# Kernel tuning notes

Hardware: AMD Instinct MI355X
Metric: run time of the kernel (lower is better)

Reference implementation:

```python
import jax, jax.numpy as jnp
import numpy as np

OBS_LEN = 8
N_PED = 2048      # total pedestrians
G = 64            # number of scenes (uniform size)
NP = N_PED // G   # pedestrians per scene = 32
H = 128           # action_decoder_hidden_dim == action_encoder_hidden_dim == f_in == f_out
DIN = 64          # action_encoder_input_dim
DD = 64           # distance_embedding_dim
NH = 4            # n_heads (hard-coded to 4 in GAT)


def setup_inputs() -> dict:
    key = jax.random.key(0)
    ks = jax.random.split(key, 16)
    s = 0.1  # weight scale (xavier-ish)
    starts = (jnp.arange(G) * NP).astype(jnp.int64)
    seq_start_end = jnp.stack([starts, starts + NP], axis=1)
    return {
        "obs_traj": jax.random.normal(ks[0], (OBS_LEN, N_PED, 2), jnp.float32),
        "goal_hidden_state": jax.random.normal(ks[1], (N_PED, H), jnp.float32),
        "goal": jax.random.normal(ks[2], (N_PED, 2), jnp.float32),
        "action": jax.random.normal(ks[3], (N_PED, 2), jnp.float32),
        "h0": jax.random.normal(ks[4], (N_PED, H), jnp.float32),
        "c0": jax.random.normal(ks[5], (N_PED, H), jnp.float32),
        "W_emb": jax.random.normal(ks[6], (2, DIN), jnp.float32) * s,
        "b_emb": jnp.zeros((DIN,), jnp.float32),
        "W_ih": jax.random.normal(ks[7], (4 * H, DIN), jnp.float32) * s,
        "W_hh": jax.random.normal(ks[8], (4 * H, H), jnp.float32) * s,
        "b_ih": jnp.zeros((4 * H,), jnp.float32),
        "b_hh": jnp.zeros((4 * H,), jnp.float32),
        "W_dist": jax.random.normal(ks[9], (8, DD), jnp.float32) * s,
        "b_dist": jnp.zeros((DD,), jnp.float32),
        "W_gate": jax.random.normal(ks[10], (DD, H), jnp.float32) * s,
        "b_gate": jnp.zeros((H,), jnp.float32),
        "gat_w": jax.random.normal(ks[11], (NH, 1, H, H), jnp.float32) * s,
        "gat_a": jax.random.normal(ks[12], (1, 1, 2 * H, 1), jnp.float32) * s,
        "gat_bias": jnp.zeros((H,), jnp.float32),
        "seq_start_end": seq_start_end,
    }


def _forward(obs_traj, goal_hidden_state, goal, action, h0, c0,
             W_emb, b_emb, W_ih, W_hh, b_ih, b_hh,
             W_dist, b_dist, W_gate, b_gate, gat_w, gat_a, gat_bias,
             seq_start_end):
    T, N, _ = obs_traj.shape
    g_num = seq_start_end.shape[0]
    n = N // g_num  # uniform group size

    # --- ActionEncoder: embed + LSTMCell loop over obs_len (lax.scan) ---
    x = jax.nn.relu(obs_traj.reshape(-1, 2) @ W_emb + b_emb).reshape(T, N, -1)

    def lstm_step(carry, xt):
        h, c = carry
        gates = xt @ W_ih.T + b_ih + h @ W_hh.T + b_hh  # torch gate order i,f,g,o
        i, f, g, o = jnp.split(gates, 4, axis=-1)
        c = jax.nn.sigmoid(f) * c + jax.nn.sigmoid(i) * jnp.tanh(g)
        h = jax.nn.sigmoid(o) * jnp.tanh(c)
        return (h, c), None

    (action_hidden, _), _ = jax.lax.scan(lstm_step, (h0, c0), x)  # [N, H]

    Hd = action_hidden.shape[-1]
    ahg = action_hidden.reshape(g_num, n, Hd)
    ghg = goal_hidden_state.reshape(g_num, n, Hd)
    glg = goal.reshape(g_num, n, 2)
    acg = action.reshape(g_num, n, 2)

    eye = jnp.eye(n, dtype=action_hidden.dtype)[:, :, None]  # [n, n, 1]

    def gat_group(ah, gh, gl, ac):
        # InteractionGate.cal_gate: dist[i,j] = [action_i, goal_i, action_j, goal_j]
        a_i = jnp.broadcast_to(ac[:, None, :], (n, n, 2))
        g_i = jnp.broadcast_to(gl[:, None, :], (n, n, 2))
        a_j = jnp.broadcast_to(ac[None, :, :], (n, n, 2))
        g_j = jnp.broadcast_to(gl[None, :, :], (n, n, 2))
        dist = jnp.concatenate([a_i, g_i, a_j, g_j], axis=-1)  # [n, n, 8]
        gate = jax.nn.sigmoid(jax.nn.relu(dist @ W_dist + b_dist) @ W_gate + b_gate)  # [n, n, H]

        # gate_action[i,j] = gate[i,j] * tanh(action_hidden[j])
        gate_action = gate * jnp.tanh(ah[None, :, :])
        # diagonal -> goal_hidden[i], off-diag -> gated action
        goal_action = eye * gh[None, :, :] + (1.0 - eye) * gate_action  # [n, n, H]

        h_other = jnp.concatenate([ah[:, None, :], goal_action], axis=1)  # [n, n+1, H]
        h_self = jnp.broadcast_to(ah[:, None, :], (n, n + 1, Hd))          # [n, n+1, H]

        # GraphAttentionLayer
        w = gat_w[:, 0]  # [NH, H, H]
        hs = jnp.einsum('nkf,hfo->hnko', h_self, w)   # [NH, n, n+1, H]
        ho = jnp.einsum('nkf,hfo->hnko', h_other, w)  # [NH, n, n+1, H]
        scores = jnp.concatenate([hs, ho], axis=-1) @ gat_a[0, 0, :, 0]  # [NH, n, n+1]
        alpha = jax.nn.softmax(jax.nn.leaky_relu(scores, 0.2), axis=-1)
        out = jnp.mean(jnp.sum(alpha[..., None] * ho, axis=2), axis=0)  # [n, H]
        return jax.nn.relu(out) + gat_bias

    out = jax.vmap(gat_group)(ahg, ghg, glg, acg)  # [G, n, H]
    return out.reshape(N, Hd)


def reference(obs_traj, goal_hidden_state, goal, action, h0, c0,
              W_emb, b_emb, W_ih, W_hh, b_ih, b_hh,
              W_dist, b_dist, W_gate, b_gate, gat_w, gat_a, gat_bias,
              seq_start_end):
    return _forward(obs_traj, goal_hidden_state, goal, action, h0, c0,
                    W_emb, b_emb, W_ih, W_hh, b_ih, b_hh,
                    W_dist, b_dist, W_gate, b_gate, gat_w, gat_a, gat_bias,
                    seq_start_end)
```

## Files before the change

kernel.cpp:

```cpp
#include <hip/hip_runtime.h>

#define N_PED 2048
#define NGROUP 64
#define NPG 32
#define HDIM 128
#define DIN 64
#define DDIM 64
#define NHEAD 4
#define TOBS 8

typedef __attribute__((ext_vector_type(8))) short bf16x8;
typedef __attribute__((ext_vector_type(4))) float f32x4;

__device__ __forceinline__ float sigm(float x){
    return __builtin_amdgcn_rcpf(1.f + __expf(-x));
}
__device__ __forceinline__ float tanh_fast(float x){
    return 1.f - 2.f*__builtin_amdgcn_rcpf(__expf(2.f*x) + 1.f);
}
__device__ __forceinline__ short f2bf(float f){
    unsigned u = __float_as_uint(f);
    unsigned r = (u + 0x7fffu + ((u >> 16) & 1u)) >> 16;
    return (short)r;
}
__device__ __forceinline__ float bf2f(unsigned short b){
    return __uint_as_float(((unsigned)b) << 16);
}
__device__ __forceinline__ unsigned pk2(float a, float b){
    return (unsigned)(unsigned short)f2bf(a) | ((unsigned)(unsigned short)f2bf(b) << 16);
}

#define WS_AHB   0
#define WS_TAHB  524288
#define WS_VW    1048576
#define WS_GF    1052672
#define WS_WF    1069056
#define WS_LF    1200128
#define WS_BSV   1396736

__global__ __launch_bounds__(512) void pack_lstm_kernel(
    const float* __restrict__ W_ih,  const float* __restrict__ W_hh,
    const float* __restrict__ b_ih,  const float* __restrict__ b_hh,
    unsigned char* __restrict__ ws)
{
    const int tid = threadIdx.x;
    const int b   = blockIdx.x;
    if (b < 24) {
        const int id = b*512 + tid;
        const int fid = id >> 6, L = id & 63;
        const int kt  = fid % 6;
        const int wi  = fid / 6;
        const int w   = wi >> 2, idx = wi & 3;
        const int q = L >> 4, ln = L & 15;
        const int n = idx*128 + w*16 + ln;
        float v[8];
        if (kt < 2) {
            const float* src = W_ih + (size_t)n*DIN + kt*32 + q*8;
            #pragma unroll
            for (int j = 0; j < 8; ++j) v[j] = src[j];
        } else {
            const float* src = W_hh + (size_t)n*HDIM + (kt-2)*32 + q*8;
            #pragma unroll
            for (int j = 0; j < 8; ++j) v[j] = src[j];
        }
        reinterpret_cast<uint4*>(ws + WS_LF)[id] =
            uint4{ pk2(v[0],v[1]), pk2(v[2],v[3]), pk2(v[4],v[5]), pk2(v[6],v[7]) };
    } else {
        ((float*)(ws + WS_BSV))[tid] = b_ih[tid] + b_hh[tid];
    }
}

#define KPAD 216
__global__ __launch_bounds__(512) void lstm_fused_kernel(
    const float* __restrict__ obs, const float* __restrict__ h0,
    const float* __restrict__ c0,  const float* __restrict__ W_emb,
    const float* __restrict__ b_emb,
    const float* __restrict__ gat_w, const float* __restrict__ gat_a,
    const float* __restrict__ W_gate,
    unsigned char* __restrict__ ws,
    unsigned short* __restrict__ AHb, unsigned short* __restrict__ TAHb)
{
    const int tid = threadIdx.x;

    if (blockIdx.x >= 256) {
        const int vb = blockIdx.x - 256;
        if (vb < 16) {
            __shared__ float sa[2*HDIM];
            __shared__ float red[32][8][2];
            float* VW = (float*)(ws + WS_VW);
            if (tid < 256) sa[tid] = gat_a[tid];
            __syncthreads();
            const int rl = (tid & 255) >> 3, ch = tid & 7;
            const int row = vb*32 + rl;
            if (tid < 256) {
                const float* rp = gat_w + (size_t)row*HDIM + ch*16;
                float v = 0.f, w1 = 0.f;
                #pragma unroll
                for (int e = 0; e < 16; ++e) {
                    float wv = rp[e];
                    v  += wv * sa[HDIM + ch*16 + e];
                    w1 += wv * sa[ch*16 + e];
                }
                red[rl][ch][0] = v; red[rl][ch][1] = w1;
            }
            __syncthreads();
            if (tid < 256 && ch == 0) {
                float sv = 0.f, sw = 0.f;
                #pragma unroll
                for (int e = 0; e < 8; ++e) { sv += red[rl][e][0]; sw += red[rl][e][1]; }
                VW[row]       = sv;
                VW[512 + row] = sw;
            }
        } else {
            const int id = (vb - 16)*512 + tid;
            if (id >= 9216) return;
            uint4* Gf4 = reinterpret_cast<uint4*>(ws + WS_GF);
            uint4* Wf4 = reinterpret_cast<uint4*>(ws + WS_WF);
            if (id < 1024) {
                const int fid = id >> 6, L = id & 63;
                const int kt = fid >> 3, nt = fid & 7;
                const int q = L >> 4, ln = L & 15;
                float v[8];
                #pragma unroll
                for (int j = 0; j < 8; ++j)
                    v[j] = W_gate[(size_t)(kt*32 + q*8 + j)*HDIM + nt*16 + ln];
                Gf4[id] = uint4{ pk2(v[0],v[1]), pk2(v[2],v[3]), pk2(v[4],v[5]), pk2(v[6],v[7]) };
            } else {
                const int id2 = id - 1024;
                const int fid = id2 >> 6, L = id2 & 63;
                const int kt = fid >> 3, nt = fid & 7;
                const int q = L >> 4, ln = L & 15;
                float v[8];
                #pragma unroll
                for (int j = 0; j < 8; ++j) {
                    int F = kt*32 + q*8 + j;
                    v[j] = gat_w[(size_t)(F >> 7)*16384 + (size_t)(F & 127)*HDIM + nt*16 + ln];
                }
                Wf4[id2] = uint4{ pk2(v[0],v[1]), pk2(v[2],v[3]), pk2(v[4],v[5]), pk2(v[6],v[7]) };
            }
        }
        return;
    }

    __shared__ short Xl[2][16][KPAD];
    __shared__ float sEmb[192];

    const int ped0 = blockIdx.x * 8;
    const int w    = tid >> 6;
    const int lane = tid & 63;
    const int q    = lane >> 4;
    const int ln   = lane & 15;
    const int u    = w*16 + ln;

    if (tid < 192) sEmb[tid] = (tid < 128) ? W_emb[tid] : b_emb[tid - 128];

    const uint4* Lf4 = reinterpret_cast<const uint4*>(ws + WS_LF);
    bf16x8 bfr[4][6];
    #pragma unroll
    for (int idx = 0; idx < 4; ++idx) {
        #pragma unroll
        for (int kt = 0; kt < 6; ++kt) {
            uint4 r = Lf4[(size_t)(((w*4 + idx)*6 + kt)*64 + lane)];
            bfr[idx][kt] = *reinterpret_cast<bf16x8*>(&r);
        }
    }
    const float* bsvp = (const float*)(ws + WS_BSV);
    float bsv[4];
    #pragma unroll
    for (int idx = 0; idx < 4; ++idx) bsv[idx] = bsvp[idx*128 + u];

    float c_st[4];
    #pragma unroll
    for (int reg = 0; reg < 4; ++reg)
        c_st[reg] = c0[(size_t)(ped0 + ((q*4 + reg) & 7))*HDIM + u];

    #pragma unroll
    for (int reg = 0; reg < 4; ++reg)
        Xl[0][q*4 + reg][64 + u] = f2bf(h0[(size_t)(ped0 + ((q*4 + reg) & 7))*HDIM + u]);
    {
        const int pr = tid >> 5, d0 = (tid & 31)*2;
        const float2 ob = reinterpret_cast<const float2*>(obs)[(size_t)(ped0 + (pr & 7))];
        float x0 = fmaxf(ob.x*sEmb[d0]   + ob.y*sEmb[64+d0]   + sEmb[128+d0],   0.f);
        float x1 = fmaxf(ob.x*sEmb[d0+1] + ob.y*sEmb[64+d0+1] + sEmb[128+d0+1], 0.f);
        *reinterpret_cast<unsigned*>(&Xl[0][pr][d0]) = pk2(x0, x1);
    }
    __syncthreads();

    float hval[4];
    for (int t = 0; t < TOBS; ++t) {
        const int cur = t & 1, nxt = cur ^ 1;

        if (t < TOBS-1) {
            const int pr = tid >> 5, d0 = (tid & 31)*2;
            const float2 ob = reinterpret_cast<const float2*>(obs)[(size_t)((t+1)*N_PED + ped0 + (pr & 7))];
            float x0 = fmaxf(ob.x*sEmb[d0]   + ob.y*sEmb[64+d0]   + sEmb[128+d0],   0.f);
            float x1 = fmaxf(ob.x*sEmb[d0+1] + ob.y*sEmb[64+d0+1] + sEmb[128+d0+1], 0.f);
            *reinterpret_cast<unsigned*>(&Xl[nxt][pr][d0]) = pk2(x0, x1);
        }

        bf16x8 afr[6];
        #pragma unroll
        for (int kt = 0; kt < 6; ++kt)
            afr[kt] = *reinterpret_cast<const bf16x8*>(&Xl[cur][ln][kt*32 + q*8]);

        f32x4 acc[4];
        #pragma unroll
        for (int idx = 0; idx < 4; ++idx) {
            f32x4 a = { bsv[idx], bsv[idx], bsv[idx], bsv[idx] };
            #pragma unroll
            for (int kt = 0; kt < 6; ++kt)
                a = __builtin_amdgcn_mfma_f32_16x16x32_bf16(afr[kt], bfr[idx][kt], a, 0, 0, 0);
            acc[idx] = a;
        }
        #pragma unroll
        for (int reg = 0; reg < 4; ++reg) {
            float c = sigm(acc[1][reg])*c_st[reg] + sigm(acc[0][reg])*tanh_fast(acc[2][reg]);
            c_st[reg] = c;
            hval[reg] = sigm(acc[3][reg])*tanh_fast(c);
        }

        if (t < TOBS-1) {
            #pragma unroll
            for (int reg = 0; reg < 4; ++reg)
                Xl[nxt][q*4 + reg][64 + u] = f2bf(hval[reg]);
            __syncthreads();
        }
    }

    if (q < 2) {
        #pragma unroll
        for (int reg = 0; reg < 4; ++reg) {
            const size_t off = (size_t)(ped0 + q*4 + reg)*HDIM + u;
            AHb[off]  = (unsigned short)f2bf(hval[reg]);
            TAHb[off] = (unsigned short)f2bf(tanh_fast(hval[reg]));
        }
    }
}

__global__ __launch_bounds__(256) void gat_kernel(
    const unsigned short* __restrict__ AHb,
    const unsigned short* __restrict__ TAHb,
    const float* __restrict__ VW,
    const unsigned char* __restrict__ ws,
    const float* __restrict__ ghs,
    const float* __restrict__ goal,
    const float* __restrict__ action,
    const float* __restrict__ W_dist,
    const float* __restrict__ b_dist,
    const float* __restrict__ b_gate,
    const float* __restrict__ gat_bias,
    float* __restrict__ out)
{
    __shared__ unsigned short sGAb[80][136];
    __shared__ unsigned short sTAHb[32][136];
    __shared__ unsigned short st1b[64][72];
    __shared__ unsigned short sU[4][520];
    __shared__ float sAl[2][4][34];
    __shared__ float sPj[80][8];
    __shared__ float sWd[8][64];
    __shared__ float sbd[64];
    __shared__ float sbg[128];
    __shared__ float sgb[128];
    __shared__ float sAC[32][2], sGL[32][2];

    const int tid = threadIdx.x;
    const int g   = blockIdx.x >> 3;
    const int i0  = (blockIdx.x & 7) * 4;
    const int p0  = g * NPG;
    const int w   = tid >> 6;
    const int L   = tid & 63;
    const int q   = L >> 4;
    const int ln  = L & 15;

    const bf16x8* Gf8 = reinterpret_cast<const bf16x8*>(ws + WS_GF);
    const bf16x8* Wf8 = reinterpret_cast<const bf16x8*>(ws + WS_WF);

    for (int s = tid; s < 512; s += 256) {
        int j = s >> 4, c = s & 15;
        *reinterpret_cast<uint4*>(&sTAHb[j][c*8]) =
            *reinterpret_cast<const uint4*>(&TAHb[(size_t)(p0 + j)*HDIM + c*8]);
    }
    if (tid < 128) {
        sbg[tid] = b_gate[tid];
        sgb[tid] = gat_bias[tid];
    } else if (tid < 192) {
        sbd[tid-128] = b_dist[tid-128];
    } else {
        int j = tid - 192;
        int pd = j & 31;
        if (j < 32) { const float2 a = reinterpret_cast<const float2*>(action)[p0+pd];
                      sAC[pd][0]=a.x; sAC[pd][1]=a.y; }
        else        { const float2 gl = reinterpret_cast<const float2*>(goal)[p0+pd];
                      sGL[pd][0]=gl.x; sGL[pd][1]=gl.y; }
    }
    if (tid < 256) {
        int rr = tid >> 6, k = tid & 63;
        sWd[rr][k]   = W_dist[rr*64 + k];
        sWd[rr+4][k] = W_dist[(rr+4)*64 + k];
    }

    bf16x8 vf[4];
    #pragma unroll
    for (int kt = 0; kt < 4; ++kt) {
        bf16x8 bb;
        #pragma unroll
        for (int j = 0; j < 8; ++j) {
            int k = kt*32 + q*8 + j;
            float v = 0.f;
            if (ln < 4)      v = VW[ln*HDIM + k];
            else if (ln < 8) v = VW[512 + (ln-4)*HDIM + k];
            bb[j] = f2bf(v);
        }
        vf[kt] = bb;
    }
    __syncthreads();

    for (int half = 0; half < 2; ++half) {
        {
            const int k = tid & 63, mg = tid >> 6;
            float base[2];
            #pragma unroll
            for (int rh = 0; rh < 2; ++rh) {
                int i = i0 + half*2 + rh;
                base[rh] = sAC[i][0]*sWd[0][k] + sAC[i][1]*sWd[1][k]
                         + sGL[i][0]*sWd[2][k] + sGL[i][1]*sWd[3][k] + sbd[k];
            }
            #pragma unroll
            for (int mm = 0; mm < 16; ++mm) {
                int m = mg*16 + mm, j = m & 31;
                float v = base[m>>5] + sAC[j][0]*sWd[4][k] + sAC[j][1]*sWd[5][k]
                                     + sGL[j][0]*sWd[6][k] + sGL[j][1]*sWd[7][k];
                st1b[m][k] = (unsigned short)f2bf(fmaxf(v, 0.f));
            }
        }
        __syncthreads();

        {
            bf16x8 afr[2];
            #pragma unroll
            for (int kt = 0; kt < 2; ++kt)
                afr[kt] = *reinterpret_cast<const bf16x8*>(&st1b[w*16 + ln][kt*32 + q*8]);
            for (int nt = 0; nt < 8; ++nt) {
                float bg = sbg[nt*16 + ln];
                f32x4 a = { bg, bg, bg, bg };
                a = __builtin_amdgcn_mfma_f32_16x16x32_bf16(afr[0], Gf8[(0*8+nt)*64 + L], a, 0, 0, 0);
                a = __builtin_amdgcn_mfma_f32_16x16x32_bf16(afr[1], Gf8[(1*8+nt)*64 + L], a, 0, 0, 0);
                #pragma unroll
                for (int reg = 0; reg < 4; ++reg) {
                    int mrow = w*16 + q*4 + reg;
                    int n = nt*16 + ln;
                    float ga = sigm(a[reg]) * bf2f(sTAHb[mrow & 31][n]);
                    sGAb[mrow][n] = (unsigned short)f2bf(ga);
                }
            }
        }
        __syncthreads();

        {
            int rh = tid >> 7, f = tid & 127;
            int irow = i0 + half*2 + rh;
            sGAb[rh*32 + irow][f] = (unsigned short)f2bf(ghs[(size_t)(p0 + irow)*HDIM + f]);
            sGAb[64 + rh][f]      = AHb[(size_t)(p0 + irow)*HDIM + f];
        }
        __syncthreads();

        {
            int nmt = (w == 0) ? 2 : 1;
            for (int e = 0; e < nmt; ++e) {
                int mt = (e == 0) ? w : 4;
                bf16x8 afr;
                f32x4 a = { 0.f, 0.f, 0.f, 0.f };
                #pragma unroll
                for (int kt = 0; kt < 4; ++kt) {
                    afr = *reinterpret_cast<const bf16x8*>(&sGAb[mt*16 + ln][kt*32 + q*8]);
                    a = __builtin_amdgcn_mfma_f32_16x16x32_bf16(afr, vf[kt], a, 0, 0, 0);
                }
                if (ln < 8) {
                    #pragma unroll
                    for (int reg = 0; reg < 4; ++reg)
                        sPj[mt*16 + q*4 + reg][ln] = a[reg];
                }
            }
        }
        __syncthreads();

        if (tid < 8) {
            int rh = tid >> 2, h = tid & 3;
            float sa_ = sPj[64 + rh][4 + h];
            float x0  = sa_ + sPj[64 + rh][h];
            x0 = (x0 < 0.f) ? 0.2f*x0 : x0;
            sAl[rh][h][0] = 1.f;
            float s0 = 1.f, s1 = 0.f, s2 = 0.f, s3 = 0.f;
            #pragma unroll
            for (int k = 1; k <= 32; k += 4) {
                float xa = sa_ + sPj[rh*32 + k - 1][h];
                float xb = sa_ + sPj[rh*32 + k    ][h];
                float xc = sa_ + sPj[rh*32 + k + 1][h];
                float xd = sa_ + sPj[rh*32 + k + 2][h];
                xa = (xa < 0.f) ? 0.2f*xa : xa;  xb = (xb < 0.f) ? 0.2f*xb : xb;
                xc = (xc < 0.f) ? 0.2f*xc : xc;  xd = (xd < 0.f) ? 0.2f*xd : xd;
                float ea = __expf(xa - x0), eb = __expf(xb - x0);
                float ec = __expf(xc - x0), ed = __expf(xd - x0);
                sAl[rh][h][k]   = ea;  sAl[rh][h][k+1] = eb;
                sAl[rh][h][k+2] = ec;  sAl[rh][h][k+3] = ed;
                s0 += ea; s1 += eb; s2 += ec; s3 += ed;
            }
            float inv = __builtin_amdgcn_rcpf((s0 + s1) + (s2 + s3));
            for (int k = 0; k <= 32; ++k) sAl[rh][h][k] *= inv;
        }
        __syncthreads();

        {
            int rh = w & 1, ntb = (w >> 1) * 4;
            int r  = half*2 + rh;
            bf16x8 afr;
            #pragma unroll
            for (int jj = 0; jj < 8; ++jj)
                afr[jj] = f2bf(sAl[rh][ln & 3][1 + q*8 + jj]);
            for (int t = 0; t < 4; ++t) {
                int nt = ntb + t;
                bf16x8 bfr;
                #pragma unroll
                for (int jj = 0; jj < 8; ++jj)
                    bfr[jj] = (short)sGAb[rh*32 + q*8 + jj][nt*16 + ln];
                f32x4 a = { 0.f, 0.f, 0.f, 0.f };
                a = __builtin_amdgcn_mfma_f32_16x16x32_bf16(afr, bfr, a, 0, 0, 0);
                if (L < 16) {
                    #pragma unroll
                    for (int reg = 0; reg < 4; ++reg) {
                        float uv = a[reg] + sAl[rh][reg][0] * bf2f(sGAb[64 + rh][nt*16 + ln]);
                        sU[r][reg*HDIM + nt*16 + ln] = (unsigned short)f2bf(uv);
                    }
                }
            }
        }
        __syncthreads();
    }

    {
        bf16x8 afr[16];
        #pragma unroll
        for (int kt = 0; kt < 16; ++kt)
            afr[kt] = *reinterpret_cast<const bf16x8*>(&sU[ln & 3][kt*32 + q*8]);
        for (int e = 0; e < 2; ++e) {
            int nt = w*2 + e;
            f32x4 a = { 0.f, 0.f, 0.f, 0.f };
            #pragma unroll
            for (int kt = 0; kt < 16; ++kt)
                a = __builtin_amdgcn_mfma_f32_16x16x32_bf16(afr[kt], Wf8[(kt*8+nt)*64 + L], a, 0, 0, 0);
            if (L < 16) {
                int o = nt*16 + ln;
                #pragma unroll
                for (int reg = 0; reg < 4; ++reg) {
                    float val = fmaxf(a[reg]*0.25f, 0.f) + sgb[o];
                    out[(size_t)(p0 + i0 + reg)*HDIM + o] = val;
                }
            }
        }
    }
}

extern "C" void kernel_launch(void* const* d_in, const int* in_sizes, int n_in,
                              void* d_out, int out_size, void* d_ws, size_t ws_size,
                              hipStream_t stream) {
    const float* obs      = (const float*)d_in[0];
    const float* ghs      = (const float*)d_in[1];
    const float* goal     = (const float*)d_in[2];
    const float* action   = (const float*)d_in[3];
    const float* h0       = (const float*)d_in[4];
    const float* c0       = (const float*)d_in[5];
    const float* W_emb    = (const float*)d_in[6];
    const float* b_emb    = (const float*)d_in[7];
    const float* W_ih     = (const float*)d_in[8];
    const float* W_hh     = (const float*)d_in[9];
    const float* b_ih     = (const float*)d_in[10];
    const float* b_hh     = (const float*)d_in[11];
    const float* W_dist   = (const float*)d_in[12];
    const float* b_dist   = (const float*)d_in[13];
    const float* W_gate   = (const float*)d_in[14];
    const float* b_gate   = (const float*)d_in[15];
    const float* gat_w    = (const float*)d_in[16];
    const float* gat_a    = (const float*)d_in[17];
    const float* gat_bias = (const float*)d_in[18];

    unsigned char* ws = (unsigned char*)d_ws;
    unsigned short* AHb  = (unsigned short*)(ws + WS_AHB);
    unsigned short* TAHb = (unsigned short*)(ws + WS_TAHB);
    float* VW            = (float*)(ws + WS_VW);
    float* out = (float*)d_out;

    hipLaunchKernelGGL(pack_lstm_kernel, dim3(25), dim3(512), 0, stream,
                       W_ih, W_hh, b_ih, b_hh, ws);
    hipLaunchKernelGGL(lstm_fused_kernel, dim3(290), dim3(512), 0, stream,
                       obs, h0, c0, W_emb, b_emb, gat_w, gat_a, W_gate, ws, AHb, TAHb);
    hipLaunchKernelGGL(gat_kernel, dim3(512), dim3(256), 0, stream,
                       AHb, TAHb, VW, ws, ghs, goal, action,
                       W_dist, b_dist, b_gate, gat_bias, out);
}
```

Before: 128.6 us.

## Precompute distance-gate sigmoid in LSTM kernel's spare blocks, store bf16 gate tensor

```diff
diff --git a/kernel.cpp b/kernel.cpp
--- a/kernel.cpp
+++ b/kernel.cpp
@@ -37,10 +37,12 @@
 #define WS_WF    1069056
 #define WS_LF    1200128
 #define WS_BSV   1396736
-
-__global__ __launch_bounds__(512) void pack_lstm_kernel(
+#define WS_GATE  1398784
+
+__global__ __launch_bounds__(512) void pack1_kernel(
     const float* __restrict__ W_ih,  const float* __restrict__ W_hh,
     const float* __restrict__ b_ih,  const float* __restrict__ b_hh,
+    const float* __restrict__ W_gate,
     unsigned char* __restrict__ ws)
 {
     const int tid = threadIdx.x;
@@ -65,8 +67,19 @@
         }
         reinterpret_cast<uint4*>(ws + WS_LF)[id] =
             uint4{ pk2(v[0],v[1]), pk2(v[2],v[3]), pk2(v[4],v[5]), pk2(v[6],v[7]) };
+    } else if (b == 24) {
+        ((float*)(ws + WS_BSV))[tid] = b_ih[tid] + b_hh[tid];
     } else {
-        ((float*)(ws + WS_BSV))[tid] = b_ih[tid] + b_hh[tid];
+        const int id = (b - 25)*512 + tid;
+        const int fid = id >> 6, L = id & 63;
+        const int kt = fid >> 3, nt = fid & 7;
+        const int q = L >> 4, ln = L & 15;
+        float v[8];
+        #pragma unroll
+        for (int j = 0; j < 8; ++j)
+            v[j] = W_gate[(size_t)(kt*32 + q*8 + j)*HDIM + nt*16 + ln];
+        reinterpret_cast<uint4*>(ws + WS_GF)[id] =
+            uint4{ pk2(v[0],v[1]), pk2(v[2],v[3]), pk2(v[4],v[5]), pk2(v[6],v[7]) };
     }
 }
 
@@ -76,7 +89,9 @@
     const float* __restrict__ c0,  const float* __restrict__ W_emb,
     const float* __restrict__ b_emb,
     const float* __restrict__ gat_w, const float* __restrict__ gat_a,
-    const float* __restrict__ W_gate,
+    const float* __restrict__ action, const float* __restrict__ goal,
+    const float* __restrict__ W_dist, const float* __restrict__ b_dist,
+    const float* __restrict__ b_gate,
     unsigned char* __restrict__ ws,
     unsigned short* __restrict__ AHb, unsigned short* __restrict__ TAHb)
 {
@@ -111,32 +126,76 @@
                 VW[row]       = sv;
                 VW[512 + row] = sw;
             }
+        } else if (vb < 32) {
+            const int id = (vb - 16)*512 + tid;
+            const int fid = id >> 6, L = id & 63;
+            const int kt = fid >> 3, nt = fid & 7;
+            const int q = L >> 4, ln = L & 15;
+            float v[8];
+            #pragma unroll
+            for (int j = 0; j < 8; ++j) {
+                int F = kt*32 + q*8 + j;
+                v[j] = gat_w[(size_t)(F >> 7)*16384 + (size_t)(F & 127)*HDIM + nt*16 + ln];
+            }
+            reinterpret_cast<uint4*>(ws + WS_WF)[id] =
+                uint4{ pk2(v[0],v[1]), pk2(v[2],v[3]), pk2(v[4],v[5]), pk2(v[6],v[7]) };
         } else {
-            const int id = (vb - 16)*512 + tid;
-            if (id >= 9216) return;
-            uint4* Gf4 = reinterpret_cast<uint4*>(ws + WS_GF);
-            uint4* Wf4 = reinterpret_cast<uint4*>(ws + WS_WF);
-            if (id < 1024) {
-                const int fid = id >> 6, L = id & 63;
-                const int kt = fid >> 3, nt = fid & 7;
-                const int q = L >> 4, ln = L & 15;
-                float v[8];
-                #pragma unroll
-                for (int j = 0; j < 8; ++j)
-                    v[j] = W_gate[(size_t)(kt*32 + q*8 + j)*HDIM + nt*16 + ln];
-                Gf4[id] = uint4{ pk2(v[0],v[1]), pk2(v[2],v[3]), pk2(v[4],v[5]), pk2(v[6],v[7]) };
-            } else {
-                const int id2 = id - 1024;
-                const int fid = id2 >> 6, L = id2 & 63;
-                const int kt = fid >> 3, nt = fid & 7;
-                const int q = L >> 4, ln = L & 15;
-                float v[8];
-                #pragma unroll
-                for (int j = 0; j < 8; ++j) {
-                    int F = kt*32 + q*8 + j;
-                    v[j] = gat_w[(size_t)(F >> 7)*16384 + (size_t)(F & 127)*HDIM + nt*16 + ln];
-                }
-                Wf4[id2] = uint4{ pk2(v[0],v[1]), pk2(v[2],v[3]), pk2(v[4],v[5]), pk2(v[6],v[7]) };
+            const int vb2 = blockIdx.x - 288;
+            const int g   = vb2 >> 2;
+            const int i0  = (vb2 & 3) * 8;
+            const int p0  = g * NPG;
+            __shared__ float gBase[8][64];
+            __shared__ float gDyn[32][64];
+            {
+                int il = tid >> 6, k = tid & 63;
+                float2 ac = reinterpret_cast<const float2*>(action)[p0 + i0 + il];
+                float2 gl = reinterpret_cast<const float2*>(goal)[p0 + i0 + il];
+                gBase[il][k] = ac.x*W_dist[k] + ac.y*W_dist[64+k]
+                             + gl.x*W_dist[128+k] + gl.y*W_dist[192+k] + b_dist[k];
+            }
+            for (int s = tid; s < 2048; s += 512) {
+                int j = s >> 6, k = s & 63;
+                float2 ac = reinterpret_cast<const float2*>(action)[p0 + j];
+                float2 gl = reinterpret_cast<const float2*>(goal)[p0 + j];
+                gDyn[j][k] = ac.x*W_dist[256+k] + ac.y*W_dist[320+k]
+                           + gl.x*W_dist[384+k] + gl.y*W_dist[448+k];
+            }
+            __syncthreads();
+            const int w  = tid >> 6;
+            const int L  = tid & 63;
+            const int q  = L >> 4;
+            const int ln = L & 15;
+            const bf16x8* Gf8 = reinterpret_cast<const bf16x8*>(ws + WS_GF);
+            unsigned short* GATE = (unsigned short*)(ws + WS_GATE);
+            #pragma unroll
+            for (int e = 0; e < 2; ++e) {
+                const int tile = w + e*8;
+                const int arow = tile*16 + ln;
+                const int ai = arow >> 5, aj = arow & 31;
+                bf16x8 afr[2];
+                #pragma unroll
+                for (int kt = 0; kt < 2; ++kt) {
+                    bf16x8 a;
+                    #pragma unroll
+                    for (int jj = 0; jj < 8; ++jj) {
+                        int k = kt*32 + q*8 + jj;
+                        a[jj] = f2bf(fmaxf(gBase[ai][k] + gDyn[aj][k], 0.f));
+                    }
+                    afr[kt] = a;
+                }
+                for (int nt = 0; nt < 8; ++nt) {
+                    float bg = b_gate[nt*16 + ln];
+                    f32x4 a = { bg, bg, bg, bg };
+                    a = __builtin_amdgcn_mfma_f32_16x16x32_bf16(afr[0], Gf8[(0*8+nt)*64 + L], a, 0, 0, 0);
+                    a = __builtin_amdgcn_mfma_f32_16x16x32_bf16(afr[1], Gf8[(1*8+nt)*64 + L], a, 0, 0, 0);
+                    #pragma unroll
+                    for (int reg = 0; reg < 4; ++reg) {
+                        int prow = tile*16 + q*4 + reg;
+                        int il = prow >> 5, jr = prow & 31;
+                        GATE[((size_t)(p0 + i0 + il)*32 + jr)*128 + nt*16 + ln] =
+                            (unsigned short)f2bf(sigm(a[reg]));
+                    }
+                }
             }
         }
         return;
@@ -243,25 +302,15 @@
     const float* __restrict__ VW,
     const unsigned char* __restrict__ ws,
     const float* __restrict__ ghs,
-    const float* __restrict__ goal,
-    const float* __restrict__ action,
-    const float* __restrict__ W_dist,
-    const float* __restrict__ b_dist,
-    const float* __restrict__ b_gate,
     const float* __restrict__ gat_bias,
     float* __restrict__ out)
 {
     __shared__ unsigned short sGAb[80][136];
     __shared__ unsigned short sTAHb[32][136];
-    __shared__ unsigned short st1b[64][72];
     __shared__ unsigned short sU[4][520];
     __shared__ float sAl[2][4][34];
     __shared__ float sPj[80][8];
-    __shared__ float sWd[8][64];
-    __shared__ float sbd[64];
-    __shared__ float sbg[128];
     __shared__ float sgb[128];
-    __shared__ float sAC[32][2], sGL[32][2];
 
     const int tid = threadIdx.x;
     const int g   = blockIdx.x >> 3;
@@ -272,32 +321,15 @@
     const int q   = L >> 4;
     const int ln  = L & 15;
 
-    const bf16x8* Gf8 = reinterpret_cast<const bf16x8*>(ws + WS_GF);
     const bf16x8* Wf8 = reinterpret_cast<const bf16x8*>(ws + WS_WF);
+    const unsigned short* GATE = (const unsigned short*)(ws + WS_GATE);
 
     for (int s = tid; s < 512; s += 256) {
         int j = s >> 4, c = s & 15;
         *reinterpret_cast<uint4*>(&sTAHb[j][c*8]) =
             *reinterpret_cast<const uint4*>(&TAHb[(size_t)(p0 + j)*HDIM + c*8]);
     }
-    if (tid < 128) {
-        sbg[tid] = b_gate[tid];
-        sgb[tid] = gat_bias[tid];
-    } else if (tid < 192) {
-        sbd[tid-128] = b_dist[tid-128];
-    } else {
-        int j = tid - 192;
-        int pd = j & 31;
-        if (j < 32) { const float2 a = reinterpret_cast<const float2*>(action)[p0+pd];
-                      sAC[pd][0]=a.x; sAC[pd][1]=a.y; }
-        else        { const float2 gl = reinterpret_cast<const float2*>(goal)[p0+pd];
-                      sGL[pd][0]=gl.x; sGL[pd][1]=gl.y; }
-    }
-    if (tid < 256) {
-        int rr = tid >> 6, k = tid & 63;
-        sWd[rr][k]   = W_dist[rr*64 + k];
-        sWd[rr+4][k] = W_dist[(rr+4)*64 + k];
-    }
+    if (tid < 128) sgb[tid] = gat_bias[tid];
 
     bf16x8 vf[4];
     #pragma unroll
@@ -316,42 +348,24 @@
     __syncthreads();
 
     for (int half = 0; half < 2; ++half) {
-        {
-            const int k = tid & 63, mg = tid >> 6;
-            float base[2];
-            #pragma unroll
-            for (int rh = 0; rh < 2; ++rh) {
-                int i = i0 + half*2 + rh;
-                base[rh] = sAC[i][0]*sWd[0][k] + sAC[i][1]*sWd[1][k]
-                         + sGL[i][0]*sWd[2][k] + sGL[i][1]*sWd[3][k] + sbd[k];
-            }
-            #pragma unroll
-            for (int mm = 0; mm < 16; ++mm) {
-                int m = mg*16 + mm, j = m & 31;
-                float v = base[m>>5] + sAC[j][0]*sWd[4][k] + sAC[j][1]*sWd[5][k]
-                                     + sGL[j][0]*sWd[6][k] + sGL[j][1]*sWd[7][k];
-                st1b[m][k] = (unsigned short)f2bf(fmaxf(v, 0.f));
-            }
-        }
-        __syncthreads();
-
-        {
-            bf16x8 afr[2];
-            #pragma unroll
-            for (int kt = 0; kt < 2; ++kt)
-                afr[kt] = *reinterpret_cast<const bf16x8*>(&st1b[w*16 + ln][kt*32 + q*8]);
-            for (int nt = 0; nt < 8; ++nt) {
-                float bg = sbg[nt*16 + ln];
-                f32x4 a = { bg, bg, bg, bg };
-                a = __builtin_amdgcn_mfma_f32_16x16x32_bf16(afr[0], Gf8[(0*8+nt)*64 + L], a, 0, 0, 0);
-                a = __builtin_amdgcn_mfma_f32_16x16x32_bf16(afr[1], Gf8[(1*8+nt)*64 + L], a, 0, 0, 0);
-                #pragma unroll
-                for (int reg = 0; reg < 4; ++reg) {
-                    int mrow = w*16 + q*4 + reg;
-                    int n = nt*16 + ln;
-                    float ga = sigm(a[reg]) * bf2f(sTAHb[mrow & 31][n]);
-                    sGAb[mrow][n] = (unsigned short)f2bf(ga);
-                }
+        #pragma unroll
+        for (int rh = 0; rh < 2; ++rh) {
+            const int irow = i0 + half*2 + rh;
+            const uint4* gp = reinterpret_cast<const uint4*>(GATE + (size_t)(p0 + irow)*32*128);
+            for (int s = tid; s < 512; s += 256) {
+                int j = s >> 4, c = s & 15;
+                uint4 gv = gp[s];
+                uint4 tv = *reinterpret_cast<const uint4*>(&sTAHb[j][c*8]);
+                unsigned r[4];
+                #pragma unroll
+                for (int e = 0; e < 4; ++e) {
+                    unsigned gu = ((const unsigned*)&gv)[e];
+                    unsigned tu = ((const unsigned*)&tv)[e];
+                    float g0 = bf2f((unsigned short)(gu & 0xffffu)) * bf2f((unsigned short)(tu & 0xffffu));
+                    float g1 = bf2f((unsigned short)(gu >> 16))     * bf2f((unsigned short)(tu >> 16));
+                    r[e] = pk2(g0, g1);
+                }
+                *reinterpret_cast<uint4*>(&sGAb[rh*32 + j][c*8]) = uint4{r[0], r[1], r[2], r[3]};
             }
         }
         __syncthreads();
@@ -489,11 +503,11 @@
     float* VW            = (float*)(ws + WS_VW);
     float* out = (float*)d_out;
 
-    hipLaunchKernelGGL(pack_lstm_kernel, dim3(25), dim3(512), 0, stream,
-                       W_ih, W_hh, b_ih, b_hh, ws);
-    hipLaunchKernelGGL(lstm_fused_kernel, dim3(290), dim3(512), 0, stream,
-                       obs, h0, c0, W_emb, b_emb, gat_w, gat_a, W_gate, ws, AHb, TAHb);
+    hipLaunchKernelGGL(pack1_kernel, dim3(27), dim3(512), 0, stream,
+                       W_ih, W_hh, b_ih, b_hh, W_gate, ws);
+    hipLaunchKernelGGL(lstm_fused_kernel, dim3(544), dim3(512), 0, stream,
+                       obs, h0, c0, W_emb, b_emb, gat_w, gat_a,
+                       action, goal, W_dist, b_dist, b_gate, ws, AHb, TAHb);
     hipLaunchKernelGGL(gat_kernel, dim3(512), dim3(256), 0, stream,
-                       AHb, TAHb, VW, ws, ghs, goal, action,
-                       W_dist, b_dist, b_gate, gat_bias, out);
-}
+                       AHb, TAHb, VW, ws, ghs, gat_bias, out);
+}
```

Measured after the change: 135.7 us. 1.06x slower.
